# Performance work log

Hardware: AMD Instinct MI355X
Metric: run time of the kernel (lower is better)

The kernel has to match this reference:

```python
import jax, jax.numpy as jnp
import numpy as np

DIM = 1024
NUM_HEADS = 16
HEAD_DIM = DIM // NUM_HEADS
B, N = 4, 2048


def _rope_sin_cos(seq_len, head_dim, dtype=jnp.float32):
    inv_freq = 1.0 / (10000.0 ** (jnp.arange(0, head_dim, 2, dtype=jnp.float32) / head_dim))
    t = jnp.arange(seq_len, dtype=jnp.float32)
    freqs = jnp.einsum('i,j->ij', t, inv_freq)          # [N, head_dim/2]
    emb = jnp.concatenate([freqs, freqs], axis=-1)      # [N, head_dim]
    return jnp.sin(emb).astype(dtype), jnp.cos(emb).astype(dtype)


def _rotate_half(x):
    x1, x2 = jnp.split(x, 2, axis=-1)
    return jnp.concatenate([-x2, x1], axis=-1)


def setup_inputs() -> dict:
    key = jax.random.key(0)
    k1, k2, k3, k4, k5 = jax.random.split(key, 5)
    scale = 0.02
    return {
        'x': jax.random.normal(k1, (B, N, DIM), dtype=jnp.float32),
        'W_qkv': jax.random.normal(k2, (DIM, 3 * DIM), dtype=jnp.float32) * scale,
        'b_qkv': jax.random.normal(k3, (3 * DIM,), dtype=jnp.float32) * scale,
        'W_proj': jax.random.normal(k4, (DIM, DIM), dtype=jnp.float32) * scale,
        'b_proj': jax.random.normal(k5, (DIM,), dtype=jnp.float32) * scale,
    }


def reference(x, W_qkv, b_qkv, W_proj, b_proj):
    Bsz, Nlen, C = x.shape
    H, Dh = NUM_HEADS, HEAD_DIM
    qkv = x @ W_qkv + b_qkv                              # [B, N, 3C]
    q, k, v = jnp.split(qkv, 3, axis=-1)
    # [B, H, N, Dh]
    q = q.reshape(Bsz, Nlen, H, Dh).transpose(0, 2, 1, 3)
    k = k.reshape(Bsz, Nlen, H, Dh).transpose(0, 2, 1, 3)
    v = v.reshape(Bsz, Nlen, H, Dh).transpose(0, 2, 1, 3)
    sin, cos = _rope_sin_cos(Nlen, Dh, x.dtype)          # [N, Dh] each, broadcast
    q = q * cos + _rotate_half(q) * sin
    k = k * cos + _rotate_half(k) * sin
    scale = 1.0 / jnp.sqrt(jnp.asarray(Dh, x.dtype))
    scores = jnp.einsum('bhqd,bhkd->bhqk', q, k) * scale  # [B, H, N, N]
    attn = jax.nn.softmax(scores, axis=-1)
    out = jnp.einsum('bhqk,bhkd->bhqd', attn, v)          # [B, H, N, Dh]
    out = out.transpose(0, 2, 1, 3).reshape(Bsz, Nlen, C)
    return out @ W_proj + b_proj
```

## Files before the change

### kernel.cpp

```cpp
#include <hip/hip_runtime.h>
#include <hip/hip_bf16.h>
#include <math.h>

#define BSZ 4
#define NSEQ 2048
#define CDIM 1024
#define NH 16
#define DH 64
#define KC 64
#define KMAX_STRIDE 32

typedef _Float16 half8_t __attribute__((ext_vector_type(8)));
typedef _Float16 half4_t __attribute__((ext_vector_type(4)));
typedef __fp16 pk2_t __attribute__((ext_vector_type(2)));
typedef __fp16 pk4_t __attribute__((ext_vector_type(4)));
typedef float floatx4 __attribute__((ext_vector_type(4)));

#define GLOBAL_AS(p) ((const __attribute__((address_space(1))) void*)(p))
#define LDS_AS(p)    ((__attribute__((address_space(3))) void*)(p))

__global__ __launch_bounds__(256) void cast_x_kernel(
    const float* __restrict__ src, _Float16* __restrict__ dst) {
  const size_t i = ((size_t)blockIdx.x * 256 + threadIdx.x) * 8;
  float4 a = *(const float4*)(src + i);
  float4 b = *(const float4*)(src + i + 4);
  half8_t h;
  h[0] = (_Float16)a.x; h[1] = (_Float16)a.y; h[2] = (_Float16)a.z; h[3] = (_Float16)a.w;
  h[4] = (_Float16)b.x; h[5] = (_Float16)b.y; h[6] = (_Float16)b.z; h[7] = (_Float16)b.w;
  *(half8_t*)(dst + i) = h;
}

__global__ __launch_bounds__(256) void transpose_cast_kernel(
    const float* __restrict__ src, _Float16* __restrict__ dst, int R, int C) {
  __shared__ float Ls[64][65];
  const int t = threadIdx.x;
  const int r0 = blockIdx.y * 64, c0 = blockIdx.x * 64;
  {
    const int lr = t >> 2, lcg = (t & 3) * 16;
    const float* s = src + (size_t)(r0 + lr) * C + c0 + lcg;
#pragma unroll
    for (int u = 0; u < 4; ++u)
      *(float4*)&Ls[lr][lcg + 4 * u] = *(const float4*)(s + 4 * u);
  }
  __syncthreads();
  const int c = t >> 2, rg = (t & 3) * 16;
  half8_t h0, h1;
#pragma unroll
  for (int u = 0; u < 8; ++u) h0[u] = (_Float16)Ls[rg + u][c];
#pragma unroll
  for (int u = 0; u < 8; ++u) h1[u] = (_Float16)Ls[rg + 8 + u][c];
  _Float16* d = dst + (size_t)(c0 + c) * R + r0 + rg;
  *(half8_t*)d = h0;
  *(half8_t*)(d + 8) = h1;
}

__global__ __launch_bounds__(256) void rope_prep_kernel(
    float2* __restrict__ tbl, unsigned* __restrict__ kmaxu) {
  const int idx = blockIdx.x * 256 + threadIdx.x;
  const int n = idx >> 5, f = idx & 31;
  const float invf = expf(-9.210340371976184f * ((float)f * (1.0f / 32.0f)));
  float s, c;
  sincosf((float)n * invf, &s, &c);
  tbl[idx] = make_float2(c, s);
  if (blockIdx.x == 0)
    for (int i = threadIdx.x; i < 64 * KMAX_STRIDE; i += 256) kmaxu[i] = 0u;
}

__global__ __launch_bounds__(256) void qkv_gemm_kernel(
    const _Float16* __restrict__ xh, const _Float16* __restrict__ Wt,
    const float* __restrict__ bias, const float2* __restrict__ rope,
    _Float16* __restrict__ Qh, _Float16* __restrict__ Kh,
    _Float16* __restrict__ Vh) {
  __shared__ _Float16 As[128 * 64];
  __shared__ _Float16 Bs[128 * 64];
  const int tid = threadIdx.x;
  const int lane = tid & 63, w = tid >> 6;
  const int m = lane & 15, quad = lane >> 4;
  const int wr = (w >> 1) * 64, wc = (w & 1) * 64;
  const int m0 = blockIdx.y * 128;
  const int N0 = blockIdx.x * 128;
  const int sr = lane >> 3, sc = (lane & 7) * 8;

  floatx4 acc[4][4];
#pragma unroll
  for (int i = 0; i < 4; ++i)
#pragma unroll
    for (int j = 0; j < 4; ++j) acc[i][j] = (floatx4){0.f, 0.f, 0.f, 0.f};

  for (int k0 = 0; k0 < CDIM; k0 += 64) {
    __syncthreads();
#pragma unroll
    for (int i = 0; i < 4; ++i) {
      const int row = (w * 4 + i) * 8 + sr;
      __builtin_amdgcn_global_load_lds(
          GLOBAL_AS(xh + (size_t)(m0 + row) * CDIM + k0 + sc),
          LDS_AS(As + (w * 4 + i) * 512), 16, 0, 0);
      __builtin_amdgcn_global_load_lds(
          GLOBAL_AS(Wt + (size_t)(N0 + row) * CDIM + k0 + sc),
          LDS_AS(Bs + (w * 4 + i) * 512), 16, 0, 0);
    }
    __syncthreads();
#pragma unroll
    for (int ks = 0; ks < 2; ++ks) {
      half8_t af[4], bf[4];
#pragma unroll
      for (int mt = 0; mt < 4; ++mt)
        af[mt] = *(half8_t*)(As + (wr + mt * 16 + m) * 64 + ks * 32 + quad * 8);
#pragma unroll
      for (int nt = 0; nt < 4; ++nt)
        bf[nt] = *(half8_t*)(Bs + (wc + nt * 16 + m) * 64 + ks * 32 + quad * 8);
#pragma unroll
      for (int mt = 0; mt < 4; ++mt)
#pragma unroll
        for (int nt = 0; nt < 4; ++nt)
          acc[mt][nt] = __builtin_amdgcn_mfma_f32_16x16x32_f16(
              af[mt], bf[nt], acc[mt][nt], 0, 0, 0);
    }
  }

  const int F0 = N0 + wc;
  const int which = F0 >> 10;
  const int head = (F0 & 1023) >> 6;
  float bv[4];
#pragma unroll
  for (int nt = 0; nt < 4; ++nt) bv[nt] = bias[F0 + nt * 16 + m];

  if (which == 2) {
#pragma unroll
    for (int mt = 0; mt < 4; ++mt)
#pragma unroll
      for (int reg = 0; reg < 4; ++reg) {
        const int gm = m0 + wr + mt * 16 + 4 * quad + reg;
        const int b = gm >> 11, n = gm & 2047;
        const size_t vbase = ((size_t)(b * NH + head) * DH) * NSEQ + n;
#pragma unroll
        for (int nt = 0; nt < 4; ++nt)
          Vh[vbase + (size_t)(nt * 16 + m) * NSEQ] =
              (_Float16)(acc[mt][nt][reg] + bv[nt]);
      }
  } else {
    _Float16* dst = which ? Kh : Qh;
    const float qs = which ? 1.0f : 0.125f * 1.4426950408889634f;
#pragma unroll
    for (int mt = 0; mt < 4; ++mt)
#pragma unroll
      for (int reg = 0; reg < 4; ++reg) {
        const int gm = m0 + wr + mt * 16 + 4 * quad + reg;
        const int b = gm >> 11, n = gm & 2047;
        const float2 csA = rope[n * 32 + m];
        const float2 csB = rope[n * 32 + 16 + m];
        const size_t obase = ((size_t)(b * NH + head) * NSEQ + n) * DH;
#pragma unroll
        for (int nt = 0; nt < 4; ++nt) {
          const float val = acc[mt][nt][reg] + bv[nt];
          const float rot = (nt < 2) ? -(acc[mt][nt + 2][reg] + bv[nt + 2])
                                     :  (acc[mt][nt - 2][reg] + bv[nt - 2]);
          const float sv = (nt & 1) ? csB.y : csA.y;
          const float cv = (nt & 1) ? csB.x : csA.x;
          dst[obase + nt * 16 + m] = (_Float16)((val * cv + rot * sv) * qs);
        }
      }
  }
}

__global__ __launch_bounds__(256) void qk_norms_kernel(
    const _Float16* __restrict__ Qh, const _Float16* __restrict__ Kh,
    float* __restrict__ qn, unsigned* __restrict__ kmaxu) {
  __shared__ float wmax[4];
  const int tid = threadIdx.x;
  const size_t row = (size_t)blockIdx.x * 32 + (tid >> 3);
  const int c = (tid & 7) * 8;
  half8_t q8 = *(const half8_t*)(Qh + row * DH + c);
  half8_t k8 = *(const half8_t*)(Kh + row * DH + c);
  float qs = 0.f, ks = 0.f;
#pragma unroll
  for (int u = 0; u < 8; ++u) {
    const float qv = (float)q8[u], kv = (float)k8[u];
    qs += qv * qv; ks += kv * kv;
  }
  qs += __shfl_xor(qs, 1, 64); ks += __shfl_xor(ks, 1, 64);
  qs += __shfl_xor(qs, 2, 64); ks += __shfl_xor(ks, 2, 64);
  qs += __shfl_xor(qs, 4, 64); ks += __shfl_xor(ks, 4, 64);
  if ((tid & 7) == 0) qn[row] = sqrtf(qs);
  ks = fmaxf(ks, __shfl_xor(ks, 8, 64));
  ks = fmaxf(ks, __shfl_xor(ks, 16, 64));
  ks = fmaxf(ks, __shfl_xor(ks, 32, 64));
  if ((tid & 63) == 0) wmax[tid >> 6] = ks;
  __syncthreads();
  if (tid == 0) {
    const float mx = fmaxf(fmaxf(wmax[0], wmax[1]), fmaxf(wmax[2], wmax[3]));
    atomicMax(&kmaxu[(row >> 11) * KMAX_STRIDE], __float_as_uint(sqrtf(mx)));
  }
}

__global__ __launch_bounds__(256) void attn_kernel(
    const _Float16* __restrict__ Qh, const _Float16* __restrict__ Kh,
    const _Float16* __restrict__ Vh, const float* __restrict__ qn,
    const unsigned* __restrict__ kmaxu, _Float16* __restrict__ AO) {
  __shared__ _Float16 smem[18432];
  float* Os = (float*)smem;

  const int tid = threadIdx.x;
  const int lane = tid & 63;
  const int w = tid >> 6;
  const int m = lane & 15;
  const int quad = lane >> 4;

  const int bid = blockIdx.x;
  const int slot = bid & 7, kk = bid >> 3;
  const int bh = slot + 8 * (kk >> 4);
  const int q0 = (kk & 15) * 128;

  const _Float16* Qb = Qh + (size_t)bh * NSEQ * DH;
  const _Float16* Kb = Kh + (size_t)bh * NSEQ * DH;
  const _Float16* Vb = Vh + (size_t)bh * DH * NSEQ;

  const int rA = q0 + w * 32 + m;
  const int rB = rA + 16;
  half8_t qfA0 = *(const half8_t*)(Qb + (size_t)rA * DH + quad * 8);
  half8_t qfA1 = *(const half8_t*)(Qb + (size_t)rA * DH + 32 + quad * 8);
  half8_t qfB0 = *(const half8_t*)(Qb + (size_t)rB * DH + quad * 8);
  half8_t qfB1 = *(const half8_t*)(Qb + (size_t)rB * DH + 32 + quad * 8);

  const float kmx = __uint_as_float(kmaxu[bh * KMAX_STRIDE]);
  const float mA = qn[(size_t)bh * NSEQ + rA] * kmx;
  const float mB = qn[(size_t)bh * NSEQ + rB] * kmx;

  const int skey = tid >> 3, sdg = (tid & 7) * 8;
  const _Float16* ksrc0 = Kb + (size_t)skey * DH + sdg;
  const _Float16* ksrc1 = Kb + (size_t)(skey + 32) * DH + sdg;
  const _Float16* vsrc0 = Vb + (size_t)skey * NSEQ + sdg;
  const _Float16* vsrc1 = Vb + (size_t)(skey + 32) * NSEQ + sdg;
  const int koff0 = skey * 72 + sdg;
  const int koff1 = (skey + 32) * 72 + sdg;

  half8_t rk0, rk1, rv0, rv1;
  auto LOAD = [&]() {
    rk0 = *(const half8_t*)ksrc0; ksrc0 += KC * DH;
    rk1 = *(const half8_t*)ksrc1; ksrc1 += KC * DH;
    rv0 = *(const half8_t*)vsrc0; vsrc0 += KC;
    rv1 = *(const half8_t*)vsrc1; vsrc1 += KC;
  };
  auto WRITE = [&](int boff) {
    _Float16* Ksb = smem + boff;
    _Float16* Vtb = smem + boff + 4608;
    *(half8_t*)(Ksb + koff0) = rk0;
    *(half8_t*)(Ksb + koff1) = rk1;
    *(half8_t*)(Vtb + koff0) = rv0;
    *(half8_t*)(Vtb + koff1) = rv1;
  };

  float lA = 0.f, lB = 0.f;
  floatx4 OA[4], OB[4];
#pragma unroll
  for (int nb = 0; nb < 4; ++nb) {
    OA[nb] = (floatx4){0.f, 0.f, 0.f, 0.f};
    OB[nb] = (floatx4){0.f, 0.f, 0.f, 0.f};
  }
  const pk2_t one2 = {(__fp16)1.f, (__fp16)1.f};

  auto COMPUTE = [&](int boff) {
    _Float16* Ks = smem + boff;
    _Float16* Vt = smem + boff + 4608;
#pragma unroll
    for (int kt = 0; kt < 4; ++kt) {
      half8_t kf0 = *(half8_t*)(Ks + (kt * 16 + m) * 72 + quad * 8);
      half8_t kf1 = *(half8_t*)(Ks + (kt * 16 + m) * 72 + 32 + quad * 8);
      __builtin_amdgcn_s_setprio(1);
      floatx4 a = (floatx4){-mA, -mA, -mA, -mA};
      a = __builtin_amdgcn_mfma_f32_16x16x32_f16(kf0, qfA0, a, 0, 0, 0);
      a = __builtin_amdgcn_mfma_f32_16x16x32_f16(kf1, qfA1, a, 0, 0, 0);
      floatx4 b = (floatx4){-mB, -mB, -mB, -mB};
      b = __builtin_amdgcn_mfma_f32_16x16x32_f16(kf0, qfB0, b, 0, 0, 0);
      b = __builtin_amdgcn_mfma_f32_16x16x32_f16(kf1, qfB1, b, 0, 0, 0);
      __builtin_amdgcn_s_setprio(0);

      const float pA0 = __builtin_exp2f(a[0]);
      const float pA1 = __builtin_exp2f(a[1]);
      const float pA2 = __builtin_exp2f(a[2]);
      const float pA3 = __builtin_exp2f(a[3]);
      const float pB0 = __builtin_exp2f(b[0]);
      const float pB1 = __builtin_exp2f(b[1]);
      const float pB2 = __builtin_exp2f(b[2]);
      const float pB3 = __builtin_exp2f(b[3]);
      pk2_t a01 = __builtin_amdgcn_cvt_pkrtz(pA0, pA1);
      pk2_t a23 = __builtin_amdgcn_cvt_pkrtz(pA2, pA3);
      pk2_t b01 = __builtin_amdgcn_cvt_pkrtz(pB0, pB1);
      pk2_t b23 = __builtin_amdgcn_cvt_pkrtz(pB2, pB3);
      lA = __builtin_amdgcn_fdot2(a01, one2, lA, false);
      lA = __builtin_amdgcn_fdot2(a23, one2, lA, false);
      lB = __builtin_amdgcn_fdot2(b01, one2, lB, false);
      lB = __builtin_amdgcn_fdot2(b23, one2, lB, false);
      half4_t phA = __builtin_bit_cast(
          half4_t, (pk4_t)__builtin_shufflevector(a01, a23, 0, 1, 2, 3));
      half4_t phB = __builtin_bit_cast(
          half4_t, (pk4_t)__builtin_shufflevector(b01, b23, 0, 1, 2, 3));

      __builtin_amdgcn_s_setprio(1);
#pragma unroll
      for (int nb = 0; nb < 4; ++nb) {
        half4_t vf = *(half4_t*)(Vt + (nb * 16 + m) * 72 + kt * 16 + quad * 4);
        OA[nb] = __builtin_amdgcn_mfma_f32_16x16x16f16(phA, vf, OA[nb], 0, 0, 0);
        OB[nb] = __builtin_amdgcn_mfma_f32_16x16x16f16(phB, vf, OB[nb], 0, 0, 0);
      }
      __builtin_amdgcn_s_setprio(0);
    }
  };

  LOAD();
  WRITE(0);
  LOAD();

  const int NCK = NSEQ / KC;
  for (int ck = 0; ck < NCK; ++ck) {
    __syncthreads();
    COMPUTE((ck & 1) * 9216);
    if (ck + 1 < NCK) {
      WRITE(((ck + 1) & 1) * 9216);
      if (ck + 2 < NCK) LOAD();
    }
  }

  lA += __shfl_xor(lA, 16, 64); lA += __shfl_xor(lA, 32, 64);
  lB += __shfl_xor(lB, 16, 64); lB += __shfl_xor(lB, 32, 64);
  float lA4[4], lB4[4];
#pragma unroll
  for (int r = 0; r < 4; ++r) {
    lA4[r] = __shfl(lA, 4 * quad + r, 64);
    lB4[r] = __shfl(lB, 4 * quad + r, 64);
  }

  const int b = bh >> 4, h = bh & 15;
  const int ql = tid >> 2, dgo = (tid & 3) * 16;
  const int gq = q0 + (ql >> 4) * 32 + (ql & 15);
  _Float16* dstA = AO + ((size_t)(b * NSEQ + gq)) * CDIM + h * DH + dgo;

  __syncthreads();
#pragma unroll
  for (int nb = 0; nb < 4; ++nb)
#pragma unroll
    for (int r = 0; r < 4; ++r)
      Os[(w * 16 + 4 * quad + r) * 68 + nb * 16 + m] = OA[nb][r] * (1.0f / lA4[r]);
  __syncthreads();
#pragma unroll
  for (int u = 0; u < 2; ++u) {
    half8_t o;
#pragma unroll
    for (int v = 0; v < 8; ++v) o[v] = (_Float16)Os[ql * 68 + dgo + u * 8 + v];
    *(half8_t*)(dstA + u * 8) = o;
  }

  __syncthreads();
#pragma unroll
  for (int nb = 0; nb < 4; ++nb)
#pragma unroll
    for (int r = 0; r < 4; ++r)
      Os[(w * 16 + 4 * quad + r) * 68 + nb * 16 + m] = OB[nb][r] * (1.0f / lB4[r]);
  __syncthreads();
  _Float16* dstB = dstA + (size_t)16 * CDIM;
#pragma unroll
  for (int u = 0; u < 2; ++u) {
    half8_t o;
#pragma unroll
    for (int v = 0; v < 8; ++v) o[v] = (_Float16)Os[ql * 68 + dgo + u * 8 + v];
    *(half8_t*)(dstB + u * 8) = o;
  }
}

__global__ __launch_bounds__(256) void proj_gemm_kernel(
    const _Float16* __restrict__ Ah, const _Float16* __restrict__ Wt,
    const float* __restrict__ bias, float* __restrict__ out) {
  __shared__ _Float16 As[128 * 64];
  __shared__ _Float16 Bs[128 * 64];
  const int tid = threadIdx.x;
  const int lane = tid & 63, w = tid >> 6;
  const int m = lane & 15, quad = lane >> 4;
  const int wr = (w >> 1) * 64, wc = (w & 1) * 64;
  const int m0 = blockIdx.y * 128;
  const int N0 = blockIdx.x * 128;
  const int sr = lane >> 3, sc = (lane & 7) * 8;

  floatx4 acc[4][4];
#pragma unroll
  for (int i = 0; i < 4; ++i)
#pragma unroll
    for (int j = 0; j < 4; ++j) acc[i][j] = (floatx4){0.f, 0.f, 0.f, 0.f};

  for (int k0 = 0; k0 < CDIM; k0 += 64) {
    __syncthreads();
#pragma unroll
    for (int i = 0; i < 4; ++i) {
      const int row = (w * 4 + i) * 8 + sr;
      __builtin_amdgcn_global_load_lds(
          GLOBAL_AS(Ah + (size_t)(m0 + row) * CDIM + k0 + sc),
          LDS_AS(As + (w * 4 + i) * 512), 16, 0, 0);
      __builtin_amdgcn_global_load_lds(
          GLOBAL_AS(Wt + (size_t)(N0 + row) * CDIM + k0 + sc),
          LDS_AS(Bs + (w * 4 + i) * 512), 16, 0, 0);
    }
    __syncthreads();
#pragma unroll
    for (int ks = 0; ks < 2; ++ks) {
      half8_t af[4], bf[4];
#pragma unroll
      for (int mt = 0; mt < 4; ++mt)
        af[mt] = *(half8_t*)(As + (wr + mt * 16 + m) * 64 + ks * 32 + quad * 8);
#pragma unroll
      for (int nt = 0; nt < 4; ++nt)
        bf[nt] = *(half8_t*)(Bs + (wc + nt * 16 + m) * 64 + ks * 32 + quad * 8);
#pragma unroll
      for (int mt = 0; mt < 4; ++mt)
#pragma unroll
        for (int nt = 0; nt < 4; ++nt)
          acc[mt][nt] = __builtin_amdgcn_mfma_f32_16x16x32_f16(
              af[mt], bf[nt], acc[mt][nt], 0, 0, 0);
    }
  }

  const int F0 = N0 + wc;
  float bv[4];
#pragma unroll
  for (int nt = 0; nt < 4; ++nt) bv[nt] = bias[F0 + nt * 16 + m];
#pragma unroll
  for (int mt = 0; mt < 4; ++mt)
#pragma unroll
    for (int reg = 0; reg < 4; ++reg) {
      const int gm = m0 + wr + mt * 16 + 4 * quad + reg;
#pragma unroll
      for (int nt = 0; nt < 4; ++nt)
        out[(size_t)gm * CDIM + F0 + nt * 16 + m] = acc[mt][nt][reg] + bv[nt];
    }
}

extern "C" void kernel_launch(void* const* d_in, const int* in_sizes, int n_in,
                              void* d_out, int out_size, void* d_ws, size_t ws_size,
                              hipStream_t stream) {
  const float* x     = (const float*)d_in[0];
  const float* Wqkv  = (const float*)d_in[1];
  const float* bqkv  = (const float*)d_in[2];
  const float* Wproj = (const float*)d_in[3];
  const float* bproj = (const float*)d_in[4];
  float* out = (float*)d_out;

  const size_t per = (size_t)BSZ * NH * NSEQ * DH;
  _Float16* xh  = (_Float16*)d_ws;
  _Float16* Wt  = xh + per;
  _Float16* Wpt = Wt + (size_t)3072 * 1024;
  _Float16* Qh  = Wpt + (size_t)1024 * 1024;
  _Float16* Kh  = Qh + per;
  _Float16* Vh  = Kh + per;
  _Float16* AOh = Vh + per;
  float*    qnp = (float*)(AOh + per);
  unsigned* kmx = (unsigned*)(qnp + (size_t)64 * NSEQ);
  float2*   ropet = (float2*)(kmx + 64 * KMAX_STRIDE);

  cast_x_kernel<<<4096, 256, 0, stream>>>(x, xh);
  transpose_cast_kernel<<<dim3(48, 16), 256, 0, stream>>>(Wqkv, Wt, 1024, 3072);
  transpose_cast_kernel<<<dim3(16, 16), 256, 0, stream>>>(Wproj, Wpt, 1024, 1024);
  rope_prep_kernel<<<256, 256, 0, stream>>>(ropet, kmx);
  qkv_gemm_kernel<<<dim3(24, 64), 256, 0, stream>>>(xh, Wt, bqkv, ropet, Qh, Kh, Vh);
  qk_norms_kernel<<<4096, 256, 0, stream>>>(Qh, Kh, qnp, kmx);
  attn_kernel<<<1024, 256, 0, stream>>>(Qh, Kh, Vh, qnp, kmx, AOh);
  proj_gemm_kernel<<<dim3(8, 64), 256, 0, stream>>>(AOh, Wpt, bproj, out);
}
```

Measured before the change: 333.4 us.

## Use 512-thread attention blocks with one 16-row tile per wave, single-buffered KV

```diff
diff --git a/kernel.cpp b/kernel.cpp
--- a/kernel.cpp
+++ b/kernel.cpp
@@ -193,12 +193,14 @@
   }
 }
 
-__global__ __launch_bounds__(256) void attn_kernel(
+__global__ __launch_bounds__(512, 8) void attn_kernel(
     const _Float16* __restrict__ Qh, const _Float16* __restrict__ Kh,
     const _Float16* __restrict__ Vh, const float* __restrict__ qn,
     const unsigned* __restrict__ kmaxu, _Float16* __restrict__ AO) {
-  __shared__ _Float16 smem[18432];
+  __shared__ _Float16 smem[17408];
   float* Os = (float*)smem;
+  _Float16* Ks = smem;
+  _Float16* Vt = smem + 4608;
 
   const int tid = threadIdx.x;
   const int lane = tid & 63;
@@ -215,53 +217,33 @@
   const _Float16* Kb = Kh + (size_t)bh * NSEQ * DH;
   const _Float16* Vb = Vh + (size_t)bh * DH * NSEQ;
 
-  const int rA = q0 + w * 32 + m;
-  const int rB = rA + 16;
+  const int rA = q0 + w * 16 + m;
   half8_t qfA0 = *(const half8_t*)(Qb + (size_t)rA * DH + quad * 8);
   half8_t qfA1 = *(const half8_t*)(Qb + (size_t)rA * DH + 32 + quad * 8);
-  half8_t qfB0 = *(const half8_t*)(Qb + (size_t)rB * DH + quad * 8);
-  half8_t qfB1 = *(const half8_t*)(Qb + (size_t)rB * DH + 32 + quad * 8);
 
   const float kmx = __uint_as_float(kmaxu[bh * KMAX_STRIDE]);
   const float mA = qn[(size_t)bh * NSEQ + rA] * kmx;
-  const float mB = qn[(size_t)bh * NSEQ + rB] * kmx;
 
   const int skey = tid >> 3, sdg = (tid & 7) * 8;
-  const _Float16* ksrc0 = Kb + (size_t)skey * DH + sdg;
-  const _Float16* ksrc1 = Kb + (size_t)(skey + 32) * DH + sdg;
-  const _Float16* vsrc0 = Vb + (size_t)skey * NSEQ + sdg;
-  const _Float16* vsrc1 = Vb + (size_t)(skey + 32) * NSEQ + sdg;
-  const int koff0 = skey * 72 + sdg;
-  const int koff1 = (skey + 32) * 72 + sdg;
-
-  half8_t rk0, rk1, rv0, rv1;
-  auto LOAD = [&]() {
-    rk0 = *(const half8_t*)ksrc0; ksrc0 += KC * DH;
-    rk1 = *(const half8_t*)ksrc1; ksrc1 += KC * DH;
-    rv0 = *(const half8_t*)vsrc0; vsrc0 += KC;
-    rv1 = *(const half8_t*)vsrc1; vsrc1 += KC;
-  };
-  auto WRITE = [&](int boff) {
-    _Float16* Ksb = smem + boff;
-    _Float16* Vtb = smem + boff + 4608;
-    *(half8_t*)(Ksb + koff0) = rk0;
-    *(half8_t*)(Ksb + koff1) = rk1;
-    *(half8_t*)(Vtb + koff0) = rv0;
-    *(half8_t*)(Vtb + koff1) = rv1;
-  };
-
-  float lA = 0.f, lB = 0.f;
-  floatx4 OA[4], OB[4];
-#pragma unroll
-  for (int nb = 0; nb < 4; ++nb) {
-    OA[nb] = (floatx4){0.f, 0.f, 0.f, 0.f};
-    OB[nb] = (floatx4){0.f, 0.f, 0.f, 0.f};
-  }
+  const _Float16* ksrc = Kb + (size_t)skey * DH + sdg;
+  const _Float16* vsrc = Vb + (size_t)skey * NSEQ + sdg;
+  const int koff = skey * 72 + sdg;
+
+  float lA = 0.f;
+  floatx4 OA[4];
+#pragma unroll
+  for (int nb = 0; nb < 4; ++nb) OA[nb] = (floatx4){0.f, 0.f, 0.f, 0.f};
   const pk2_t one2 = {(__fp16)1.f, (__fp16)1.f};
 
-  auto COMPUTE = [&](int boff) {
-    _Float16* Ks = smem + boff;
-    _Float16* Vt = smem + boff + 4608;
+  const int NCK = NSEQ / KC;
+  for (int ck = 0; ck < NCK; ++ck) {
+    half8_t k8 = *(const half8_t*)ksrc;  ksrc += KC * DH;
+    half8_t v8 = *(const half8_t*)vsrc;  vsrc += KC;
+    __syncthreads();
+    *(half8_t*)(Ks + koff) = k8;
+    *(half8_t*)(Vt + koff) = v8;
+    __syncthreads();
+
 #pragma unroll
     for (int kt = 0; kt < 4; ++kt) {
       half8_t kf0 = *(half8_t*)(Ks + (kt * 16 + m) * 72 + quad * 8);
@@ -270,70 +252,36 @@
       floatx4 a = (floatx4){-mA, -mA, -mA, -mA};
       a = __builtin_amdgcn_mfma_f32_16x16x32_f16(kf0, qfA0, a, 0, 0, 0);
       a = __builtin_amdgcn_mfma_f32_16x16x32_f16(kf1, qfA1, a, 0, 0, 0);
-      floatx4 b = (floatx4){-mB, -mB, -mB, -mB};
-      b = __builtin_amdgcn_mfma_f32_16x16x32_f16(kf0, qfB0, b, 0, 0, 0);
-      b = __builtin_amdgcn_mfma_f32_16x16x32_f16(kf1, qfB1, b, 0, 0, 0);
       __builtin_amdgcn_s_setprio(0);
 
-      const float pA0 = __builtin_exp2f(a[0]);
-      const float pA1 = __builtin_exp2f(a[1]);
-      const float pA2 = __builtin_exp2f(a[2]);
-      const float pA3 = __builtin_exp2f(a[3]);
-      const float pB0 = __builtin_exp2f(b[0]);
-      const float pB1 = __builtin_exp2f(b[1]);
-      const float pB2 = __builtin_exp2f(b[2]);
-      const float pB3 = __builtin_exp2f(b[3]);
-      pk2_t a01 = __builtin_amdgcn_cvt_pkrtz(pA0, pA1);
-      pk2_t a23 = __builtin_amdgcn_cvt_pkrtz(pA2, pA3);
-      pk2_t b01 = __builtin_amdgcn_cvt_pkrtz(pB0, pB1);
-      pk2_t b23 = __builtin_amdgcn_cvt_pkrtz(pB2, pB3);
+      pk2_t a01 = __builtin_amdgcn_cvt_pkrtz(__builtin_exp2f(a[0]),
+                                             __builtin_exp2f(a[1]));
+      pk2_t a23 = __builtin_amdgcn_cvt_pkrtz(__builtin_exp2f(a[2]),
+                                             __builtin_exp2f(a[3]));
       lA = __builtin_amdgcn_fdot2(a01, one2, lA, false);
       lA = __builtin_amdgcn_fdot2(a23, one2, lA, false);
-      lB = __builtin_amdgcn_fdot2(b01, one2, lB, false);
-      lB = __builtin_amdgcn_fdot2(b23, one2, lB, false);
       half4_t phA = __builtin_bit_cast(
           half4_t, (pk4_t)__builtin_shufflevector(a01, a23, 0, 1, 2, 3));
-      half4_t phB = __builtin_bit_cast(
-          half4_t, (pk4_t)__builtin_shufflevector(b01, b23, 0, 1, 2, 3));
 
       __builtin_amdgcn_s_setprio(1);
 #pragma unroll
       for (int nb = 0; nb < 4; ++nb) {
         half4_t vf = *(half4_t*)(Vt + (nb * 16 + m) * 72 + kt * 16 + quad * 4);
         OA[nb] = __builtin_amdgcn_mfma_f32_16x16x16f16(phA, vf, OA[nb], 0, 0, 0);
-        OB[nb] = __builtin_amdgcn_mfma_f32_16x16x16f16(phB, vf, OB[nb], 0, 0, 0);
       }
       __builtin_amdgcn_s_setprio(0);
     }
-  };
-
-  LOAD();
-  WRITE(0);
-  LOAD();
-
-  const int NCK = NSEQ / KC;
-  for (int ck = 0; ck < NCK; ++ck) {
-    __syncthreads();
-    COMPUTE((ck & 1) * 9216);
-    if (ck + 1 < NCK) {
-      WRITE(((ck + 1) & 1) * 9216);
-      if (ck + 2 < NCK) LOAD();
-    }
   }
 
   lA += __shfl_xor(lA, 16, 64); lA += __shfl_xor(lA, 32, 64);
-  lB += __shfl_xor(lB, 16, 64); lB += __shfl_xor(lB, 32, 64);
-  float lA4[4], lB4[4];
-#pragma unroll
-  for (int r = 0; r < 4; ++r) {
-    lA4[r] = __shfl(lA, 4 * quad + r, 64);
-    lB4[r] = __shfl(lB, 4 * quad + r, 64);
-  }
+  float lA4[4];
+#pragma unroll
+  for (int r = 0; r < 4; ++r) lA4[r] = __shfl(lA, 4 * quad + r, 64);
 
   const int b = bh >> 4, h = bh & 15;
   const int ql = tid >> 2, dgo = (tid & 3) * 16;
-  const int gq = q0 + (ql >> 4) * 32 + (ql & 15);
-  _Float16* dstA = AO + ((size_t)(b * NSEQ + gq)) * CDIM + h * DH + dgo;
+  const int gq = q0 + ql;
+  _Float16* dst = AO + ((size_t)(b * NSEQ + gq)) * CDIM + h * DH + dgo;
 
   __syncthreads();
 #pragma unroll
@@ -347,23 +295,7 @@
     half8_t o;
 #pragma unroll
     for (int v = 0; v < 8; ++v) o[v] = (_Float16)Os[ql * 68 + dgo + u * 8 + v];
-    *(half8_t*)(dstA + u * 8) = o;
-  }
-
-  __syncthreads();
-#pragma unroll
-  for (int nb = 0; nb < 4; ++nb)
-#pragma unroll
-    for (int r = 0; r < 4; ++r)
-      Os[(w * 16 + 4 * quad + r) * 68 + nb * 16 + m] = OB[nb][r] * (1.0f / lB4[r]);
-  __syncthreads();
-  _Float16* dstB = dstA + (size_t)16 * CDIM;
-#pragma unroll
-  for (int u = 0; u < 2; ++u) {
-    half8_t o;
-#pragma unroll
-    for (int v = 0; v < 8; ++v) o[v] = (_Float16)Os[ql * 68 + dgo + u * 8 + v];
-    *(half8_t*)(dstB + u * 8) = o;
+    *(half8_t*)(dst + u * 8) = o;
   }
 }
 
@@ -460,6 +392,6 @@
   rope_prep_kernel<<<256, 256, 0, stream>>>(ropet, kmx);
   qkv_gemm_kernel<<<dim3(24, 64), 256, 0, stream>>>(xh, Wt, bqkv, ropet, Qh, Kh, Vh);
   qk_norms_kernel<<<4096, 256, 0, stream>>>(Qh, Kh, qnp, kmx);
-  attn_kernel<<<1024, 256, 0, stream>>>(Qh, Kh, Vh, qnp, kmx, AOh);
+  attn_kernel<<<1024, 512, 0, stream>>>(Qh, Kh, Vh, qnp, kmx, AOh);
   proj_gemm_kernel<<<dim3(8, 64), 256, 0, stream>>>(AOh, Wpt, bproj, out);
 }
```

Result: faster. 319.3 us (-4.2%).
